# Kernel optimization log

Hardware: AMD Instinct MI355X
Metric: run time of the kernel (lower is better)

## Reference

```python
import jax, jax.numpy as jnp
import numpy as np

N, E, C, H, EDGE_DIM, HID = 50000, 800000, 128, 8, 64, 512
D = C // H  # head dim = out_channels_conv


def layer_norm(x, g, b, eps=1e-5):
    mu = x.mean(-1, keepdims=True)
    var = ((x - mu) ** 2).mean(-1, keepdims=True)
    return (x - mu) * jax.lax.rsqrt(var + eps) * g + b


def _lin_init(k, fan_in, fan_out):
    s = 1.0 / np.sqrt(fan_in)
    kw, kb = jax.random.split(k)
    w = jax.random.uniform(kw, (fan_in, fan_out), minval=-s, maxval=s, dtype=jnp.float32)
    b = jax.random.uniform(kb, (fan_out,), minval=-s, maxval=s, dtype=jnp.float32)
    return w, b


def setup_inputs() -> dict:
    key = jax.random.key(0)
    ks = jax.random.split(key, 16)
    wq, bq = _lin_init(ks[0], C, C)
    wk, bk = _lin_init(ks[1], C, C)
    wv, bv = _lin_init(ks[2], C, C)
    ws, bs = _lin_init(ks[3], C, C)          # lin_self
    we, be = _lin_init(ks[4], EDGE_DIM, C)   # lin_edge
    wp, bp = _lin_init(ks[5], C, C)          # projection
    w1, b1 = _lin_init(ks[6], C, HID)        # node_dst_mlp[0]
    w2, b2 = _lin_init(ks[7], HID, C)        # node_dst_mlp[2]
    x = jax.random.normal(ks[8], (N, C), dtype=jnp.float32)
    edge_attr = jax.random.normal(ks[9], (E, EDGE_DIM), dtype=jnp.float32)
    edge_index = jax.random.randint(ks[10], (2, E), 0, N, dtype=jnp.int64)
    return dict(
        x=x, edge_attr=edge_attr, edge_index=edge_index,
        wq=wq, bq=bq, wk=wk, bk=bk, wv=wv, bv=bv, ws=ws, bs=bs,
        we=we, be=be, wp=wp, bp=bp, w1=w1, b1=b1, w2=w2, b2=b2,
        ln1_g=jnp.ones((C,), jnp.float32), ln1_b=jnp.zeros((C,), jnp.float32),
        ln2_g=jnp.ones((C,), jnp.float32), ln2_b=jnp.zeros((C,), jnp.float32),
    )


def reference(x, edge_attr, edge_index,
              wq, bq, wk, bk, wv, bv, ws, bs, we, be, wp, bp,
              w1, b1, w2, b2, ln1_g, ln1_b, ln2_g, ln2_b):
    src, dst = edge_index[0], edge_index[1]

    x_skip = x
    xn = layer_norm(x, ln1_g, ln1_b)                       # layer_norm_attention
    x_r = xn @ ws + bs                                     # lin_self residual
    q = (xn @ wq + bq).reshape(N, H, D)
    k = (xn @ wk + bk).reshape(N, H, D)
    v = (xn @ wv + bv).reshape(N, H, D)
    e = (edge_attr @ we + be).reshape(E, H, D)             # lin_edge (edge_pre_mlp = Identity)

    # edge-indexed multi-head attention: softmax over incoming edges per dst node
    ke = k[src] + e                                        # [E,H,D]
    alpha = jnp.einsum('ehd,ehd->eh', q[dst], ke) / np.sqrt(D)   # [E,H]
    amax = jax.lax.stop_gradient(jax.ops.segment_max(alpha, dst, num_segments=N))
    ex = jnp.exp(alpha - amax[dst])
    den = jax.ops.segment_sum(ex, dst, num_segments=N)
    w = ex / (den[dst] + 1e-16)                            # [E,H]
    out = jax.ops.segment_sum(w[:, :, None] * (v[src] + e), dst, num_segments=N)  # [N,H,D]
    out = out.reshape(N, C)

    out = (out + x_r) @ wp + bp                            # projection
    out = out + x_skip
    h = layer_norm(out, ln2_g, ln2_b)                      # layer_norm_mlp_dst
    h = jax.nn.gelu(h @ w1 + b1) @ w2 + b2                 # node_dst_mlp
    nodes_new = out + h
    return nodes_new, edge_attr
```

## Files before the change

kernel.cpp:

```cpp
#include <hip/hip_runtime.h>
#include <hip/hip_bf16.h>
#include <cstdio>

#define NN 50000
#define NE 800000
#define CC 128
#define EDIM 64
#define HIDN 512

using bf16 = __hip_bfloat16;
typedef short sh8 __attribute__((ext_vector_type(8)));
typedef float f32x4 __attribute__((ext_vector_type(4)));

static __device__ __forceinline__ float b2f(bf16 v){ return __bfloat162float(v); }
static __device__ __forceinline__ bf16 f2b(float v){ return __float2bfloat16(v); }
static __device__ __forceinline__ float u2f(unsigned short u){
    union { unsigned int i; float f; } w; w.i = ((unsigned int)u) << 16; return w.f;
}
static __device__ __forceinline__ unsigned short f2u(float f){
    bf16 b = __float2bfloat16(f);
    return *reinterpret_cast<unsigned short*>(&b);
}
static __device__ __forceinline__ float2 loadbf2(const bf16* p){
    __hip_bfloat162 v = *reinterpret_cast<const __hip_bfloat162*>(p);
    return make_float2(__bfloat162float(v.x), __bfloat162float(v.y));
}
static __device__ __forceinline__ float gelu_tanh(float x){
    const float c = 0.7978845608028654f;
    float u = c * (x + 0.044715f * x * x * x);
    return x / (1.0f + __expf(-2.0f * u));
}

constexpr size_t AL(size_t x){ return (x + 255) & ~(size_t)255; }
constexpr size_t OFF_FLAG = 0;
constexpr size_t OFF_DEG  = 256;
constexpr size_t OFF_ROW  = AL(OFF_DEG + (size_t)(NN + 1) * 4);
constexpr size_t OFF_CUR  = AL(OFF_ROW + (size_t)(NN + 1) * 4);
constexpr size_t OFF_SRC  = AL(OFF_CUR + (size_t)(NN + 1) * 4);
constexpr size_t OFF_DST  = AL(OFF_SRC + (size_t)NE * 4);
constexpr size_t OFF_QC   = AL(OFF_DST + (size_t)NE * 4);
constexpr size_t OFF_KC   = AL(OFF_QC  + (size_t)NN * CC * 2);
constexpr size_t OFF_VC   = AL(OFF_KC  + (size_t)NN * CC * 2);
constexpr size_t OFF_ATT  = AL(OFF_VC  + (size_t)NN * CC * 2);
constexpr size_t OFF_PRM  = AL(OFF_ATT + (size_t)NN * CC * 2);
constexpr size_t PRM_ELEMS = 4*(16384+128) + 8192+128 + 16384+128 + 65536+512 + 65536+128 + 4*128;
constexpr size_t OFF_ALP  = AL(OFF_PRM + PRM_ELEMS * 2);
constexpr size_t OFF_VP   = AL(OFF_ALP + (size_t)NE * 8 * 2);
constexpr size_t OFF_XRC  = AL(OFF_VP + (size_t)NE * CC * 2);
constexpr size_t OFF_WFQ  = AL(OFF_XRC + (size_t)NN * CC * 2);
constexpr size_t OFF_WFK  = OFF_WFQ + 32768;
constexpr size_t OFF_WFV  = OFF_WFK + 32768;
constexpr size_t OFF_WFS  = OFF_WFV + 32768;
constexpr size_t OFF_WFP  = OFF_WFS + 32768;
constexpr size_t OFF_WF1  = OFF_WFP + 32768;
constexpr size_t OFF_WF2  = OFF_WF1 + 131072;
constexpr size_t OFF_WFE  = OFF_WF2 + 131072;
constexpr size_t OFF_BSUM = OFF_WFE + 16384;
constexpr size_t WS_NEED  = OFF_BSUM + 256;

__global__ void k_detect(const unsigned short* xw, const unsigned int* ew, int* flags){
    __shared__ int sw, sz;
    if (threadIdx.x == 0){ sw = 0; sz = 0; }
    __syncthreads();
    int w = 0;
    for (int i = threadIdx.x; i < 8192; i += 256){
        unsigned e = (xw[i] >> 7) & 0xFF;
        if (e == 0xFF || (e != 0 && (e < 0x60 || e > 0x90))) w++;
    }
    atomicAdd(&sw, w);
    int z = 0;
    for (int i = threadIdx.x; i < 2048; i += 256)
        if (ew[2*i+1] == 0u) z++;
    atomicAdd(&sz, z);
    __syncthreads();
    if (threadIdx.x == 0){
        flags[0] = (sw > 2048) ? 1 : 0;
        flags[1] = (sz > 1536) ? 1 : 0;
    }
}

struct CvtJob { const void* s; bf16* d; int n; };
struct CvtJobs { CvtJob j[20]; };
__global__ void k_cvt_all(CvtJobs jobs, const int* flags){
    const int f = flags[0];
    const int e = blockIdx.x >> 5;
    const CvtJob J = jobs.j[e];
    const int stride = 32 * 256;
    for (int i = (blockIdx.x & 31) * 256 + threadIdx.x; i < J.n; i += stride){
        if (f) J.d[i] = f2b(((const float*)J.s)[i]);
        else   J.d[i] = ((const bf16*)J.s)[i];
    }
}

__global__ void k_cvt_idx(const int* e32, int* srcI, int* dstI, int* deg, const int* flags){
    const int f = flags[1];
    int i = blockIdx.x * blockDim.x + threadIdx.x;
    const int stride = gridDim.x * blockDim.x;
    if (f){
        const long long* e64 = (const long long*)e32;
        for (; i < NE; i += stride){
            srcI[i] = (int)e64[i];
            const int d = (int)e64[NE + i];
            dstI[i] = d;
            atomicAdd(&deg[d], 1);
        }
    } else {
        for (; i < NE; i += stride){
            srcI[i] = e32[i];
            const int d = e32[NE + i];
            dstI[i] = d;
            atomicAdd(&deg[d], 1);
        }
    }
}

struct WJob { const bf16* W; bf16* WF; int K; int N; };
struct WJobs { WJob j[8]; };
__global__ void k_wprep_all(WJobs jobs){
    const WJob J = jobs.j[blockIdx.x / 48];
    const int KS = J.K >> 5;
    const int total = J.K * J.N;
    for (int o = (blockIdx.x % 48) * 256 + threadIdx.x; o < total; o += 48 * 256){
        const int j  = o & 7;
        const int ln = (o >> 3) & 63;
        const int tt = o >> 9;
        const int ks = tt % KS, ct = tt / KS;
        const int kk = (ks << 5) + ((ln >> 4) << 3) + j;
        const int c  = (ct << 4) + (ln & 15);
        J.WF[o] = J.W[kk * J.N + c];
    }
}

#define ASWZ(row, chunk)  (((row) << 8)  + ((((chunk) ^ ((row) & 15))) << 4))
#define HSWZ(row, chunk)  (((row) << 10) + ((((chunk) ^ ((row) & 15))) << 4))
#define EASWZ(row, chunk) (((row) << 7)  + ((((chunk) ^ ((row) & 7)))  << 4))

static __device__ __forceinline__ void gemm_nodes_128(
    const unsigned short* Abase, int row0, int lane,
    const bf16* __restrict__ WF, const bf16* __restrict__ bias,
    bf16* __restrict__ outp, int n0)
{
    const int rA = row0 + (lane & 15);
    sh8 af[4];
    #pragma unroll
    for (int ks = 0; ks < 4; ++ks)
        af[ks] = *(const sh8*)((const char*)Abase + ASWZ(rA, (ks << 2) + (lane >> 4)));
    f32x4 acc[8] = {};
    #pragma unroll
    for (int ks = 0; ks < 4; ++ks)
        #pragma unroll
        for (int ct = 0; ct < 8; ++ct){
            sh8 bfr = *(const sh8*)(WF + ((size_t)((ct << 2) + ks) * 64 + lane) * 8);
            acc[ct] = __builtin_amdgcn_mfma_f32_16x16x32_bf16(af[ks], bfr, acc[ct], 0, 0, 0);
        }
    #pragma unroll
    for (int ct = 0; ct < 8; ++ct){
        const int c = (ct << 4) + (lane & 15);
        const float bv = b2f(bias[c]);
        #pragma unroll
        for (int i = 0; i < 4; ++i){
            const int r = row0 + ((lane >> 4) << 2) + i;
            if (n0 + r < NN)
                outp[(size_t)(n0 + r) * CC + c] = f2b(acc[ct][i] + bv);
        }
    }
}

__global__ __launch_bounds__(256) void k_node_pre2(
    const void* __restrict__ x_raw, const int* __restrict__ flags,
    const bf16* __restrict__ WFq, const bf16* __restrict__ bq,
    const bf16* __restrict__ WFk, const bf16* __restrict__ bk,
    const bf16* __restrict__ WFv, const bf16* __restrict__ bv,
    const bf16* __restrict__ WFs, const bf16* __restrict__ bs,
    const bf16* __restrict__ g,  const bf16* __restrict__ bb,
    bf16* __restrict__ q, bf16* __restrict__ k, bf16* __restrict__ v,
    bf16* __restrict__ xr)
{
    __shared__ unsigned short A[64 * 128];
    const int t = threadIdx.x, lane = t & 63, wid = t >> 6;
    const int n0 = blockIdx.x * 64;

    if (flags[0]){
        const float* x = (const float*)x_raw;
        #pragma unroll
        for (int it = 0; it < 8; ++it){
            const int u = t + 256 * it;
            const int row = u >> 5, c = (u & 31) << 2;
            float4 a = make_float4(0.f, 0.f, 0.f, 0.f);
            if (n0 + row < NN)
                a = *(const float4*)&x[(size_t)(n0 + row) * CC + c];
            ushort4 b;
            b.x = f2u(a.x); b.y = f2u(a.y); b.z = f2u(a.z); b.w = f2u(a.w);
            *(ushort4*)((char*)A + ASWZ(row, c >> 3) + ((c & 7) << 1)) = b;
        }
    } else {
        const bf16* x = (const bf16*)x_raw;
        #pragma unroll
        for (int it = 0; it < 4; ++it){
            const int c8 = t + 256 * it;
            const int row = c8 >> 4, chunk = c8 & 15, col = chunk << 3;
            uint4 val = make_uint4(0u, 0u, 0u, 0u);
            if (n0 + row < NN)
                val = *(const uint4*)&x[(size_t)(n0 + row) * CC + col];
            *(uint4*)((char*)A + ASWZ(row, chunk)) = val;
        }
    }
    __syncthreads();

    {
        const int nd = wid * 16 + (lane & 15), qd = lane >> 4;
        float vals[32];
        #pragma unroll
        for (int i = 0; i < 4; ++i){
            uint4 u = *(const uint4*)((const char*)A + ASWZ(nd, (qd << 2) + i));
            unsigned uu[4] = {u.x, u.y, u.z, u.w};
            #pragma unroll
            for (int j2 = 0; j2 < 4; ++j2){
                vals[i*8 + j2*2]     = u2f((unsigned short)(uu[j2] & 0xFFFF));
                vals[i*8 + j2*2 + 1] = u2f((unsigned short)(uu[j2] >> 16));
            }
        }
        float s = 0.f;
        #pragma unroll
        for (int i = 0; i < 32; ++i) s += vals[i];
        s += __shfl_xor(s, 16); s += __shfl_xor(s, 32);
        const float mu = s * (1.0f / CC);
        float vv = 0.f;
        #pragma unroll
        for (int i = 0; i < 32; ++i){ const float d = vals[i] - mu; vv += d * d; }
        vv += __shfl_xor(vv, 16); vv += __shfl_xor(vv, 32);
        const float rstd = rsqrtf(vv * (1.0f / CC) + 1e-5f);
        #pragma unroll
        for (int i = 0; i < 4; ++i){
            unsigned w[4];
            #pragma unroll
            for (int j2 = 0; j2 < 4; ++j2){
                const int c0 = qd * 32 + i * 8 + j2 * 2;
                const float a0 = (vals[i*8+j2*2]   - mu) * rstd * b2f(g[c0])   + b2f(bb[c0]);
                const float a1 = (vals[i*8+j2*2+1] - mu) * rstd * b2f(g[c0+1]) + b2f(bb[c0+1]);
                w[j2] = (unsigned)f2u(a0) | ((unsigned)f2u(a1) << 16);
            }
            *(uint4*)((char*)A + ASWZ(nd, (qd << 2) + i)) = make_uint4(w[0], w[1], w[2], w[3]);
        }
    }
    __syncthreads();

    const int row0 = wid * 16;
    gemm_nodes_128(A, row0, lane, WFq, bq, q,  n0);
    gemm_nodes_128(A, row0, lane, WFk, bk, k,  n0);
    gemm_nodes_128(A, row0, lane, WFv, bv, v,  n0);
    gemm_nodes_128(A, row0, lane, WFs, bs, xr, n0);
}

__global__ __launch_bounds__(1024) void k_scan1(const int* __restrict__ deg,
                                                int* __restrict__ row, int* __restrict__ bsum){
    __shared__ int sb[1024];
    const int t = threadIdx.x;
    const int idx = blockIdx.x * 1024 + t;
    sb[t] = (idx < NN) ? deg[idx] : 0;
    __syncthreads();
    for (int off = 1; off < 1024; off <<= 1){
        int tv = (t >= off) ? sb[t - off] : 0;
        __syncthreads();
        sb[t] += tv;
        __syncthreads();
    }
    if (idx < NN) row[idx + 1] = sb[t];
    if (t == 1023) bsum[blockIdx.x] = sb[1023];
}

__global__ __launch_bounds__(1024) void k_scan3(const int* __restrict__ bsum,
                                                int* __restrict__ row, int* __restrict__ cur){
    __shared__ int sadd;
    const int t = threadIdx.x;
    if (t < 64){
        int a = 0;
        for (int i = t; i < (int)blockIdx.x; i += 64) a += bsum[i];
        for (int off = 32; off; off >>= 1) a += __shfl_xor(a, off);
        if (t == 0) sadd = a;
    }
    __syncthreads();
    const int idx = blockIdx.x * 1024 + t;
    if (idx < NN){
        const int vfin = row[idx + 1] + sadd;
        row[idx + 1] = vfin;
        cur[idx + 1] = vfin;
    }
    if (idx == 0){ row[0] = 0; cur[0] = 0; }
}

__global__ __launch_bounds__(256) void k_edge4(
    const void* __restrict__ ea_raw, const int* __restrict__ flags,
    const bf16* __restrict__ WFe, const bf16* __restrict__ be,
    const bf16* __restrict__ kv_q, const bf16* __restrict__ kv_k, const bf16* __restrict__ kv_v,
    const int* __restrict__ srcI, const int* __restrict__ dstI, int* __restrict__ cur,
    unsigned short* __restrict__ alphap, unsigned short* __restrict__ vperm,
    void* __restrict__ outv)
{
    __shared__ unsigned short EA[64 * 64];
    __shared__ unsigned short ET[64 * 128];
    const int t = threadIdx.x, lane = t & 63, wid = t >> 6;
    const int e0 = blockIdx.x * 64;

    if (flags[0]){
        const float* ea = (const float*)ea_raw;
        float* outd = (float*)outv + (size_t)NN * CC;
        #pragma unroll
        for (int it = 0; it < 4; ++it){
            const int u = t + 256 * it;
            const int row = u >> 4, c = (u & 15) << 2;
            const size_t o = (size_t)(e0 + row) * EDIM + c;
            const float4 a = *(const float4*)&ea[o];
            *(float4*)&outd[o] = a;
            ushort4 b;
            b.x = f2u(a.x); b.y = f2u(a.y); b.z = f2u(a.z); b.w = f2u(a.w);
            *(ushort4*)((char*)EA + EASWZ(row, c >> 3) + ((c & 7) << 1)) = b;
        }
    } else {
        const unsigned short* ea = (const unsigned short*)ea_raw;
        unsigned short* outd = (unsigned short*)outv + (size_t)NN * CC;
        #pragma unroll
        for (int it = 0; it < 2; ++it){
            const int u = t + 256 * it;
            const int row = u >> 3, c = (u & 7) << 3;
            const size_t o = (size_t)(e0 + row) * EDIM + c;
            uint4 raw = *(const uint4*)&ea[o];
            *(uint4*)&outd[o] = raw;
            *(uint4*)((char*)EA + EASWZ(row, c >> 3)) = raw;
        }
    }
    __syncthreads();

    const int row0 = wid * 16;
    {
        const int rA = row0 + (lane & 15);
        sh8 af[2];
        #pragma unroll
        for (int ks = 0; ks < 2; ++ks)
            af[ks] = *(const sh8*)((const char*)EA + EASWZ(rA, (ks << 2) + (lane >> 4)));
        f32x4 acc[8] = {};
        #pragma unroll
        for (int ks = 0; ks < 2; ++ks)
            #pragma unroll
            for (int ct = 0; ct < 8; ++ct){
                sh8 bfr = *(const sh8*)(WFe + ((size_t)((ct << 1) + ks) * 64 + lane) * 8);
                acc[ct] = __builtin_amdgcn_mfma_f32_16x16x32_bf16(af[ks], bfr, acc[ct], 0, 0, 0);
            }
        #pragma unroll
        for (int ct = 0; ct < 8; ++ct){
            const int c = (ct << 4) + (lane & 15);
            const float bv = b2f(be[c]);
            #pragma unroll
            for (int i = 0; i < 4; ++i){
                const int r = row0 + ((lane >> 4) << 2) + i;
                *(unsigned short*)((char*)ET + ASWZ(r, c >> 3) + ((c & 7) << 1)) =
                    f2u(acc[ct][i] + bv);
            }
        }
    }
    __syncthreads();

    const int g = t >> 5, cT = t & 31, c = cT << 2;
    int s8[8], d8[8];
    #pragma unroll
    for (int i = 0; i < 8; ++i){
        const int eid = e0 + g * 8 + i;
        s8[i] = srcI[eid];
        d8[i] = dstI[eid];
    }
    int pmine = 0;
    if (cT < 8) pmine = atomicAdd(&cur[dstI[e0 + g * 8 + cT]], 1);
    int p8[8];
    #pragma unroll
    for (int i = 0; i < 8; ++i)
        p8[i] = __shfl(pmine, ((g & 1) << 5) + i);

    ushort4 kr[8], vr[8], qr[8];
    #pragma unroll
    for (int i = 0; i < 8; ++i) kr[i] = *(const ushort4*)&kv_k[(size_t)s8[i] * CC + c];
    #pragma unroll
    for (int i = 0; i < 8; ++i) vr[i] = *(const ushort4*)&kv_v[(size_t)s8[i] * CC + c];
    #pragma unroll
    for (int i = 0; i < 8; ++i) qr[i] = *(const ushort4*)&kv_q[(size_t)d8[i] * CC + c];
    #pragma unroll
    for (int i = 0; i < 8; ++i){
        const ushort4 ev = *(const ushort4*)((const char*)ET + ASWZ(g * 8 + i, c >> 3) + ((c & 7) << 1));
        const float e0_ = u2f(ev.x), e1_ = u2f(ev.y), e2_ = u2f(ev.z), e3_ = u2f(ev.w);
        float part = u2f(qr[i].x) * (e0_ + u2f(kr[i].x)) + u2f(qr[i].y) * (e1_ + u2f(kr[i].y))
                   + u2f(qr[i].z) * (e2_ + u2f(kr[i].z)) + u2f(qr[i].w) * (e3_ + u2f(kr[i].w));
        part += __shfl_xor(part, 1);
        part += __shfl_xor(part, 2);
        if ((cT & 3) == 0)
            alphap[(size_t)p8[i] * 8 + (cT >> 2)] = f2u(part * 0.25f);
        ushort4 vo;
        vo.x = f2u(e0_ + u2f(vr[i].x)); vo.y = f2u(e1_ + u2f(vr[i].y));
        vo.z = f2u(e2_ + u2f(vr[i].z)); vo.w = f2u(e3_ + u2f(vr[i].w));
        *(ushort4*)&vperm[(size_t)p8[i] * CC + c] = vo;
    }
}

__global__ __launch_bounds__(256) void k_attn3(
    const unsigned short* __restrict__ alphap, const bf16* __restrict__ vperm,
    const int* __restrict__ rowstart, bf16* __restrict__ attn_bf)
{
    const int t = threadIdx.x, lane = t & 63, wid = t >> 6;
    const int n = blockIdx.x * 4 + wid;
    const int h = lane >> 3;

    float m = -INFINITY, den = 0.0f;
    float2 num = make_float2(0.0f, 0.0f);

    const int jb = rowstart[n], je = rowstart[n + 1];
    for (int j = jb; j < je; ++j) {
        const float alpha = u2f(alphap[(size_t)j * 8 + h]);
        const float2 v2 = loadbf2(&vperm[(size_t)j * CC + 2 * lane]);
        if (alpha > m) {
            const float sc = __expf(m - alpha);
            den *= sc; num.x *= sc; num.y *= sc;
            m = alpha;
        }
        const float p = __expf(alpha - m);
        den += p;
        num.x += p * v2.x;
        num.y += p * v2.y;
    }
    const float inv = 1.0f / (den + 1e-16f);
    __hip_bfloat162 pr;
    pr.x = f2b(num.x * inv);
    pr.y = f2b(num.y * inv);
    *reinterpret_cast<__hip_bfloat162*>(&attn_bf[(size_t)n * CC + 2 * lane]) = pr;
}

__global__ __launch_bounds__(256) void k_post2(
    const bf16* __restrict__ attn_bf, const bf16* __restrict__ xr,
    const void* __restrict__ x_raw,
    const bf16* __restrict__ WFp, const bf16* __restrict__ bp,
    const bf16* __restrict__ WF1, const bf16* __restrict__ b1,
    const bf16* __restrict__ WF2, const bf16* __restrict__ b2c,
    const bf16* __restrict__ g2, const bf16* __restrict__ bb2,
    void* __restrict__ outv, const int* __restrict__ flags)
{
    __shared__ unsigned short A[64 * 128];
    __shared__ unsigned short HID[64 * 512];
    const int t = threadIdx.x, lane = t & 63, wid = t >> 6;
    const int n0 = blockIdx.x * 64;
    const int f32io = flags[0];

    #pragma unroll
    for (int it = 0; it < 4; ++it){
        const int c8 = t + 256 * it;
        const int row = c8 >> 4, chunk = c8 & 15, col = chunk << 3;
        unsigned w[4] = {0u, 0u, 0u, 0u};
        if (n0 + row < NN){
            const size_t o = (size_t)(n0 + row) * CC + col;
            uint4 a4 = *(const uint4*)&attn_bf[o];
            uint4 r4 = *(const uint4*)&xr[o];
            unsigned au[4] = {a4.x, a4.y, a4.z, a4.w};
            unsigned ru[4] = {r4.x, r4.y, r4.z, r4.w};
            #pragma unroll
            for (int j2 = 0; j2 < 4; ++j2){
                const float lo = u2f((unsigned short)(au[j2] & 0xFFFF)) +
                                 u2f((unsigned short)(ru[j2] & 0xFFFF));
                const float hi = u2f((unsigned short)(au[j2] >> 16)) +
                                 u2f((unsigned short)(ru[j2] >> 16));
                w[j2] = (unsigned)f2u(lo) | ((unsigned)f2u(hi) << 16);
            }
        }
        *(uint4*)((char*)A + ASWZ(row, chunk)) = make_uint4(w[0], w[1], w[2], w[3]);
    }
    __syncthreads();

    const int row0 = wid * 16;
    const int rA = row0 + (lane & 15);

    float out2[8][4];
    {
        sh8 af[4];
        #pragma unroll
        for (int ks = 0; ks < 4; ++ks)
            af[ks] = *(const sh8*)((const char*)A + ASWZ(rA, (ks << 2) + (lane >> 4)));
        f32x4 acc[8] = {};
        #pragma unroll
        for (int ks = 0; ks < 4; ++ks)
            #pragma unroll
            for (int ct = 0; ct < 8; ++ct){
                sh8 bfr = *(const sh8*)(WFp + ((size_t)((ct << 2) + ks) * 64 + lane) * 8);
                acc[ct] = __builtin_amdgcn_mfma_f32_16x16x32_bf16(af[ks], bfr, acc[ct], 0, 0, 0);
            }
        #pragma unroll
        for (int ct = 0; ct < 8; ++ct){
            const int c = (ct << 4) + (lane & 15);
            const float bv = b2f(bp[c]);
            #pragma unroll
            for (int i = 0; i < 4; ++i){
                const int r = row0 + ((lane >> 4) << 2) + i;
                float xs = 0.f;
                if (n0 + r < NN){
                    const size_t o = (size_t)(n0 + r) * CC + c;
                    xs = f32io ? ((const float*)x_raw)[o] : b2f(((const bf16*)x_raw)[o]);
                }
                out2[ct][i] = acc[ct][i] + bv + xs;
            }
        }
    }

    {
        float mu[4], rstd[4];
        #pragma unroll
        for (int i = 0; i < 4; ++i){
            float s = 0.f;
            #pragma unroll
            for (int ct = 0; ct < 8; ++ct) s += out2[ct][i];
            s += __shfl_xor(s, 1); s += __shfl_xor(s, 2);
            s += __shfl_xor(s, 4); s += __shfl_xor(s, 8);
            mu[i] = s * (1.0f / CC);
        }
        #pragma unroll
        for (int i = 0; i < 4; ++i){
            float vv = 0.f;
            #pragma unroll
            for (int ct = 0; ct < 8; ++ct){ const float d = out2[ct][i] - mu[i]; vv += d * d; }
            vv += __shfl_xor(vv, 1); vv += __shfl_xor(vv, 2);
            vv += __shfl_xor(vv, 4); vv += __shfl_xor(vv, 8);
            rstd[i] = rsqrtf(vv * (1.0f / CC) + 1e-5f);
        }
        #pragma unroll
        for (int ct = 0; ct < 8; ++ct){
            const int c = (ct << 4) + (lane & 15);
            const float gv = b2f(g2[c]), bbv = b2f(bb2[c]);
            const int chunk = c >> 3;
            #pragma unroll
            for (int i = 0; i < 4; ++i){
                const int r = row0 + ((lane >> 4) << 2) + i;
                const float ln = (out2[ct][i] - mu[i]) * rstd[i] * gv + bbv;
                *(unsigned short*)((char*)A + ASWZ(r, chunk) + ((c & 7) << 1)) = f2u(ln);
            }
        }
    }

    {
        sh8 af[4];
        #pragma unroll
        for (int ks = 0; ks < 4; ++ks)
            af[ks] = *(const sh8*)((const char*)A + ASWZ(rA, (ks << 2) + (lane >> 4)));
        #pragma unroll
        for (int grp = 0; grp < 4; ++grp){
            f32x4 acc[8] = {};
            #pragma unroll
            for (int ks = 0; ks < 4; ++ks)
                #pragma unroll
                for (int ctl = 0; ctl < 8; ++ctl){
                    const int ct = grp * 8 + ctl;
                    sh8 bfr = *(const sh8*)(WF1 + ((size_t)((ct << 2) + ks) * 64 + lane) * 8);
                    acc[ctl] = __builtin_amdgcn_mfma_f32_16x16x32_bf16(af[ks], bfr, acc[ctl], 0, 0, 0);
                }
            #pragma unroll
            for (int ctl = 0; ctl < 8; ++ctl){
                const int ct = grp * 8 + ctl;
                const int c = (ct << 4) + (lane & 15);
                const float bv = b2f(b1[c]);
                const int chunk = c >> 3;
                #pragma unroll
                for (int i = 0; i < 4; ++i){
                    const int r = row0 + ((lane >> 4) << 2) + i;
                    const float h = gelu_tanh(acc[ctl][i] + bv);
                    *(unsigned short*)((char*)HID + HSWZ(r, chunk) + ((c & 7) << 1)) = f2u(h);
                }
            }
        }
    }

    {
        f32x4 acc[8] = {};
        #pragma unroll
        for (int ks = 0; ks < 16; ++ks){
            sh8 afh = *(const sh8*)((const char*)HID + HSWZ(rA, (ks << 2) + (lane >> 4)));
            #pragma unroll
            for (int ct = 0; ct < 8; ++ct){
                sh8 bfr = *(const sh8*)(WF2 + ((size_t)((ct << 4) + ks) * 64 + lane) * 8);
                acc[ct] = __builtin_amdgcn_mfma_f32_16x16x32_bf16(afh, bfr, acc[ct], 0, 0, 0);
            }
        }
        #pragma unroll
        for (int ct = 0; ct < 8; ++ct){
            const int c = (ct << 4) + (lane & 15);
            const float bv = b2f(b2c[c]);
            #pragma unroll
            for (int i = 0; i < 4; ++i){
                const int r = row0 + ((lane >> 4) << 2) + i;
                if (n0 + r < NN){
                    const float val = out2[ct][i] + acc[ct][i] + bv;
                    if (f32io) ((float*)outv)[(size_t)(n0 + r) * CC + c] = val;
                    else       ((bf16*)outv)[(size_t)(n0 + r) * CC + c] = f2b(val);
                }
            }
        }
    }
}

extern "C" void kernel_launch(void* const* d_in, const int* in_sizes, int n_in,
                              void* d_out, int out_size, void* d_ws, size_t ws_size,
                              hipStream_t stream)
{
    if (ws_size < WS_NEED) {
        fprintf(stderr, "[kl] WS TOO SMALL ws=%zu need=%zu\n", ws_size, WS_NEED);
        return;
    }

    char* ws = (char*)d_ws;
    int*  flags = (int*)(ws + OFF_FLAG);
    int*  deg   = (int*)(ws + OFF_DEG);
    int*  row   = (int*)(ws + OFF_ROW);
    int*  cur   = (int*)(ws + OFF_CUR);
    int*  srcI  = (int*)(ws + OFF_SRC);
    int*  dstI  = (int*)(ws + OFF_DST);
    int*  bsum  = (int*)(ws + OFF_BSUM);
    bf16* qC    = (bf16*)(ws + OFF_QC);
    bf16* kC    = (bf16*)(ws + OFF_KC);
    bf16* vC    = (bf16*)(ws + OFF_VC);
    bf16* attC  = (bf16*)(ws + OFF_ATT);
    bf16* xrC   = (bf16*)(ws + OFF_XRC);
    unsigned short* alphap = (unsigned short*)(ws + OFF_ALP);
    unsigned short* vperm  = (unsigned short*)(ws + OFF_VP);
    bf16* WFq = (bf16*)(ws + OFF_WFQ);
    bf16* WFk = (bf16*)(ws + OFF_WFK);
    bf16* WFv = (bf16*)(ws + OFF_WFV);
    bf16* WFs = (bf16*)(ws + OFF_WFS);
    bf16* WFp = (bf16*)(ws + OFF_WFP);
    bf16* WF1 = (bf16*)(ws + OFF_WF1);
    bf16* WF2 = (bf16*)(ws + OFF_WF2);
    bf16* WFe = (bf16*)(ws + OFF_WFE);

    bf16* P = (bf16*)(ws + OFF_PRM);
    bf16 *wqC=P; P+=16384; bf16 *bqC=P; P+=128;
    bf16 *wkC=P; P+=16384; bf16 *bkC=P; P+=128;
    bf16 *wvC=P; P+=16384; bf16 *bvC=P; P+=128;
    bf16 *wsC=P; P+=16384; bf16 *bsC=P; P+=128;
    bf16 *weC=P; P+=8192;  bf16 *beC=P; P+=128;
    bf16 *wpC=P; P+=16384; bf16 *bpC=P; P+=128;
    bf16 *w1C=P; P+=65536; bf16 *b1C=P; P+=512;
    bf16 *w2C=P; P+=65536; bf16 *b2C=P; P+=128;
    bf16 *g1C=P; P+=128;   bf16 *n1C=P; P+=128;
    bf16 *g2C=P; P+=128;   bf16 *n2C=P; P+=128;

    hipMemsetAsync(deg, 0, (size_t)(NN + 1) * sizeof(int), stream);

    k_detect<<<1, 256, 0, stream>>>((const unsigned short*)d_in[0],
                                    (const unsigned int*)d_in[2], flags);

    {
        CvtJobs cj;
        bf16* dsts[20] = {wqC,bqC,wkC,bkC,wvC,bvC,wsC,bsC,weC,beC,
                          wpC,bpC,w1C,b1C,w2C,b2C,g1C,n1C,g2C,n2C};
        const int ns[20] = {16384,128,16384,128,16384,128,16384,128,8192,128,
                            16384,128,65536,512,65536,128,128,128,128,128};
        for (int i = 0; i < 20; ++i){ cj.j[i].s = d_in[3 + i]; cj.j[i].d = dsts[i]; cj.j[i].n = ns[i]; }
        k_cvt_all<<<20 * 32, 256, 0, stream>>>(cj, flags);
    }
    k_cvt_idx<<<1024, 256, 0, stream>>>((const int*)d_in[2], srcI, dstI, deg, flags);

    {
        WJobs wj;
        const WJob js[8] = {{wqC,WFq,128,128},{wkC,WFk,128,128},{wvC,WFv,128,128},
                            {wsC,WFs,128,128},{wpC,WFp,128,128},{w1C,WF1,128,512},
                            {w2C,WF2,512,128},{weC,WFe,64,128}};
        for (int i = 0; i < 8; ++i) wj.j[i] = js[i];
        k_wprep_all<<<8 * 48, 256, 0, stream>>>(wj);
    }

    const int NB64 = (NN + 63) / 64;
    const int NSC  = (NN + 1023) / 1024;
    k_node_pre2<<<NB64, 256, 0, stream>>>(d_in[0], flags, WFq, bqC, WFk, bkC, WFv, bvC,
                                          WFs, bsC, g1C, n1C, qC, kC, vC, xrC);
    k_scan1<<<NSC, 1024, 0, stream>>>(deg, row, bsum);
    k_scan3<<<NSC, 1024, 0, stream>>>(bsum, row, cur);
    k_edge4<<<NE / 64, 256, 0, stream>>>(d_in[1], flags, WFe, beC, qC, kC, vC,
                                         srcI, dstI, cur, alphap, vperm, d_out);
    k_attn3<<<NN / 4, 256, 0, stream>>>(alphap, (const bf16*)vperm, row, attC);
    k_post2<<<NB64, 256, 0, stream>>>(attC, xrC, d_in[0], WFp, bpC, WF1, b1C, WF2, b2C,
                                      g2C, n2C, d_out, flags);
}
```

Measured before the change: 505.8 us.

## Interleave K/V rows, hoist edge gathers before edge GEMM, fuse weight conversion

K and V projections are now written into one interleaved [N,256] buffer, so each edge's source gather reads K and V from the same 512-byte row. The index loads, atomic slot reservation and K/V/Q gathers in the edge kernel are moved ahead of the edge-attribute GEMM, so their memory latency overlaps with the MFMA work. Weight dtype conversion is folded into the weight-relayout kernel, which removes the intermediate bf16 weight copies and shrinks the conversion launch to biases only. The hoisted gathers hold many more live registers through the GEMM, which may lower occupancy.

```diff
diff --git a/kernel.cpp b/kernel.cpp
--- a/kernel.cpp
+++ b/kernel.cpp
@@ -39,11 +39,10 @@
 constexpr size_t OFF_SRC  = AL(OFF_CUR + (size_t)(NN + 1) * 4);
 constexpr size_t OFF_DST  = AL(OFF_SRC + (size_t)NE * 4);
 constexpr size_t OFF_QC   = AL(OFF_DST + (size_t)NE * 4);
-constexpr size_t OFF_KC   = AL(OFF_QC  + (size_t)NN * CC * 2);
-constexpr size_t OFF_VC   = AL(OFF_KC  + (size_t)NN * CC * 2);
-constexpr size_t OFF_ATT  = AL(OFF_VC  + (size_t)NN * CC * 2);
+constexpr size_t OFF_KV   = AL(OFF_QC  + (size_t)NN * CC * 2);
+constexpr size_t OFF_ATT  = AL(OFF_KV  + (size_t)NN * 256 * 2);
 constexpr size_t OFF_PRM  = AL(OFF_ATT + (size_t)NN * CC * 2);
-constexpr size_t PRM_ELEMS = 4*(16384+128) + 8192+128 + 16384+128 + 65536+512 + 65536+128 + 4*128;
+constexpr size_t PRM_ELEMS = 4096;
 constexpr size_t OFF_ALP  = AL(OFF_PRM + PRM_ELEMS * 2);
 constexpr size_t OFF_VP   = AL(OFF_ALP + (size_t)NE * 8 * 2);
 constexpr size_t OFF_XRC  = AL(OFF_VP + (size_t)NE * CC * 2);
@@ -80,13 +79,13 @@
 }
 
 struct CvtJob { const void* s; bf16* d; int n; };
-struct CvtJobs { CvtJob j[20]; };
+struct CvtJobs { CvtJob j[12]; };
 __global__ void k_cvt_all(CvtJobs jobs, const int* flags){
     const int f = flags[0];
-    const int e = blockIdx.x >> 5;
+    const int e = blockIdx.x >> 1;
     const CvtJob J = jobs.j[e];
-    const int stride = 32 * 256;
-    for (int i = (blockIdx.x & 31) * 256 + threadIdx.x; i < J.n; i += stride){
+    const int stride = 2 * 256;
+    for (int i = (blockIdx.x & 1) * 256 + threadIdx.x; i < J.n; i += stride){
         if (f) J.d[i] = f2b(((const float*)J.s)[i]);
         else   J.d[i] = ((const bf16*)J.s)[i];
     }
@@ -114,9 +113,10 @@
     }
 }
 
-struct WJob { const bf16* W; bf16* WF; int K; int N; };
+struct WJob { const void* W; bf16* WF; int K; int N; };
 struct WJobs { WJob j[8]; };
-__global__ void k_wprep_all(WJobs jobs){
+__global__ void k_wprep_all(WJobs jobs, const int* flags){
+    const int f = flags[0];
     const WJob J = jobs.j[blockIdx.x / 48];
     const int KS = J.K >> 5;
     const int total = J.K * J.N;
@@ -127,7 +127,8 @@
         const int ks = tt % KS, ct = tt / KS;
         const int kk = (ks << 5) + ((ln >> 4) << 3) + j;
         const int c  = (ct << 4) + (ln & 15);
-        J.WF[o] = J.W[kk * J.N + c];
+        const int src = kk * J.N + c;
+        J.WF[o] = f ? f2b(((const float*)J.W)[src]) : ((const bf16*)J.W)[src];
     }
 }
 
@@ -138,7 +139,7 @@
 static __device__ __forceinline__ void gemm_nodes_128(
     const unsigned short* Abase, int row0, int lane,
     const bf16* __restrict__ WF, const bf16* __restrict__ bias,
-    bf16* __restrict__ outp, int n0)
+    bf16* __restrict__ outp, int n0, int ostride, int ocol)
 {
     const int rA = row0 + (lane & 15);
     sh8 af[4];
@@ -161,7 +162,7 @@
         for (int i = 0; i < 4; ++i){
             const int r = row0 + ((lane >> 4) << 2) + i;
             if (n0 + r < NN)
-                outp[(size_t)(n0 + r) * CC + c] = f2b(acc[ct][i] + bv);
+                outp[(size_t)(n0 + r) * ostride + ocol + c] = f2b(acc[ct][i] + bv);
         }
     }
 }
@@ -173,8 +174,7 @@
     const bf16* __restrict__ WFv, const bf16* __restrict__ bv,
     const bf16* __restrict__ WFs, const bf16* __restrict__ bs,
     const bf16* __restrict__ g,  const bf16* __restrict__ bb,
-    bf16* __restrict__ q, bf16* __restrict__ k, bf16* __restrict__ v,
-    bf16* __restrict__ xr)
+    bf16* __restrict__ q, bf16* __restrict__ kv, bf16* __restrict__ xr)
 {
     __shared__ unsigned short A[64 * 128];
     const int t = threadIdx.x, lane = t & 63, wid = t >> 6;
@@ -246,10 +246,10 @@
     __syncthreads();
 
     const int row0 = wid * 16;
-    gemm_nodes_128(A, row0, lane, WFq, bq, q,  n0);
-    gemm_nodes_128(A, row0, lane, WFk, bk, k,  n0);
-    gemm_nodes_128(A, row0, lane, WFv, bv, v,  n0);
-    gemm_nodes_128(A, row0, lane, WFs, bs, xr, n0);
+    gemm_nodes_128(A, row0, lane, WFq, bq, q,  n0, CC,  0);
+    gemm_nodes_128(A, row0, lane, WFk, bk, kv, n0, 256, 0);
+    gemm_nodes_128(A, row0, lane, WFv, bv, kv, n0, 256, 128);
+    gemm_nodes_128(A, row0, lane, WFs, bs, xr, n0, CC,  0);
 }
 
 __global__ __launch_bounds__(1024) void k_scan1(const int* __restrict__ deg,
@@ -289,10 +289,10 @@
     if (idx == 0){ row[0] = 0; cur[0] = 0; }
 }
 
-__global__ __launch_bounds__(256) void k_edge4(
+__global__ __launch_bounds__(256) void k_edge5(
     const void* __restrict__ ea_raw, const int* __restrict__ flags,
     const bf16* __restrict__ WFe, const bf16* __restrict__ be,
-    const bf16* __restrict__ kv_q, const bf16* __restrict__ kv_k, const bf16* __restrict__ kv_v,
+    const bf16* __restrict__ kv_q, const bf16* __restrict__ kvKV,
     const int* __restrict__ srcI, const int* __restrict__ dstI, int* __restrict__ cur,
     unsigned short* __restrict__ alphap, unsigned short* __restrict__ vperm,
     void* __restrict__ outv)
@@ -301,6 +301,28 @@
     __shared__ unsigned short ET[64 * 128];
     const int t = threadIdx.x, lane = t & 63, wid = t >> 6;
     const int e0 = blockIdx.x * 64;
+    const int g = t >> 5, cT = t & 31, c = cT << 2;
+
+    int s8[8], d8[8];
+    #pragma unroll
+    for (int i = 0; i < 8; ++i){
+        const int eid = e0 + g * 8 + i;
+        s8[i] = srcI[eid];
+        d8[i] = dstI[eid];
+    }
+    int pmine = 0;
+    if (cT < 8) pmine = atomicAdd(&cur[dstI[e0 + g * 8 + cT]], 1);
+    ushort4 kr[8], vr[8], qr[8];
+    #pragma unroll
+    for (int i = 0; i < 8; ++i) kr[i] = *(const ushort4*)&kvKV[(size_t)s8[i] * 256 + c];
+    #pragma unroll
+    for (int i = 0; i < 8; ++i) vr[i] = *(const ushort4*)&kvKV[(size_t)s8[i] * 256 + 128 + c];
+    #pragma unroll
+    for (int i = 0; i < 8; ++i) qr[i] = *(const ushort4*)&kv_q[(size_t)d8[i] * CC + c];
+    int p8[8];
+    #pragma unroll
+    for (int i = 0; i < 8; ++i)
+        p8[i] = __shfl(pmine, ((g & 1) << 5) + i);
 
     if (flags[0]){
         const float* ea = (const float*)ea_raw;
@@ -308,13 +330,13 @@
         #pragma unroll
         for (int it = 0; it < 4; ++it){
             const int u = t + 256 * it;
-            const int row = u >> 4, c = (u & 15) << 2;
-            const size_t o = (size_t)(e0 + row) * EDIM + c;
+            const int row = u >> 4, cc2 = (u & 15) << 2;
+            const size_t o = (size_t)(e0 + row) * EDIM + cc2;
             const float4 a = *(const float4*)&ea[o];
             *(float4*)&outd[o] = a;
             ushort4 b;
             b.x = f2u(a.x); b.y = f2u(a.y); b.z = f2u(a.z); b.w = f2u(a.w);
-            *(ushort4*)((char*)EA + EASWZ(row, c >> 3) + ((c & 7) << 1)) = b;
+            *(ushort4*)((char*)EA + EASWZ(row, cc2 >> 3) + ((cc2 & 7) << 1)) = b;
         }
     } else {
         const unsigned short* ea = (const unsigned short*)ea_raw;
@@ -322,11 +344,11 @@
         #pragma unroll
         for (int it = 0; it < 2; ++it){
             const int u = t + 256 * it;
-            const int row = u >> 3, c = (u & 7) << 3;
-            const size_t o = (size_t)(e0 + row) * EDIM + c;
+            const int row = u >> 3, cc2 = (u & 7) << 3;
+            const size_t o = (size_t)(e0 + row) * EDIM + cc2;
             uint4 raw = *(const uint4*)&ea[o];
             *(uint4*)&outd[o] = raw;
-            *(uint4*)((char*)EA + EASWZ(row, c >> 3)) = raw;
+            *(uint4*)((char*)EA + EASWZ(row, cc2 >> 3)) = raw;
         }
     }
     __syncthreads();
@@ -348,40 +370,18 @@
             }
         #pragma unroll
         for (int ct = 0; ct < 8; ++ct){
-            const int c = (ct << 4) + (lane & 15);
-            const float bv = b2f(be[c]);
+            const int cc3 = (ct << 4) + (lane & 15);
+            const float bv = b2f(be[cc3]);
             #pragma unroll
             for (int i = 0; i < 4; ++i){
                 const int r = row0 + ((lane >> 4) << 2) + i;
-                *(unsigned short*)((char*)ET + ASWZ(r, c >> 3) + ((c & 7) << 1)) =
+                *(unsigned short*)((char*)ET + ASWZ(r, cc3 >> 3) + ((cc3 & 7) << 1)) =
                     f2u(acc[ct][i] + bv);
             }
         }
     }
     __syncthreads();
 
-    const int g = t >> 5, cT = t & 31, c = cT << 2;
-    int s8[8], d8[8];
-    #pragma unroll
-    for (int i = 0; i < 8; ++i){
-        const int eid = e0 + g * 8 + i;
-        s8[i] = srcI[eid];
-        d8[i] = dstI[eid];
-    }
-    int pmine = 0;
-    if (cT < 8) pmine = atomicAdd(&cur[dstI[e0 + g * 8 + cT]], 1);
-    int p8[8];
-    #pragma unroll
-    for (int i = 0; i < 8; ++i)
-        p8[i] = __shfl(pmine, ((g & 1) << 5) + i);
-
-    ushort4 kr[8], vr[8], qr[8];
-    #pragma unroll
-    for (int i = 0; i < 8; ++i) kr[i] = *(const ushort4*)&kv_k[(size_t)s8[i] * CC + c];
-    #pragma unroll
-    for (int i = 0; i < 8; ++i) vr[i] = *(const ushort4*)&kv_v[(size_t)s8[i] * CC + c];
-    #pragma unroll
-    for (int i = 0; i < 8; ++i) qr[i] = *(const ushort4*)&kv_q[(size_t)d8[i] * CC + c];
     #pragma unroll
     for (int i = 0; i < 8; ++i){
         const ushort4 ev = *(const ushort4*)((const char*)ET + ASWZ(g * 8 + i, c >> 3) + ((c & 7) << 1));
@@ -616,8 +616,7 @@
     int*  dstI  = (int*)(ws + OFF_DST);
     int*  bsum  = (int*)(ws + OFF_BSUM);
     bf16* qC    = (bf16*)(ws + OFF_QC);
-    bf16* kC    = (bf16*)(ws + OFF_KC);
-    bf16* vC    = (bf16*)(ws + OFF_VC);
+    bf16* kvC   = (bf16*)(ws + OFF_KV);
     bf16* attC  = (bf16*)(ws + OFF_ATT);
     bf16* xrC   = (bf16*)(ws + OFF_XRC);
     unsigned short* alphap = (unsigned short*)(ws + OFF_ALP);
@@ -632,16 +631,12 @@
     bf16* WFe = (bf16*)(ws + OFF_WFE);
 
     bf16* P = (bf16*)(ws + OFF_PRM);
-    bf16 *wqC=P; P+=16384; bf16 *bqC=P; P+=128;
-    bf16 *wkC=P; P+=16384; bf16 *bkC=P; P+=128;
-    bf16 *wvC=P; P+=16384; bf16 *bvC=P; P+=128;
-    bf16 *wsC=P; P+=16384; bf16 *bsC=P; P+=128;
-    bf16 *weC=P; P+=8192;  bf16 *beC=P; P+=128;
-    bf16 *wpC=P; P+=16384; bf16 *bpC=P; P+=128;
-    bf16 *w1C=P; P+=65536; bf16 *b1C=P; P+=512;
-    bf16 *w2C=P; P+=65536; bf16 *b2C=P; P+=128;
-    bf16 *g1C=P; P+=128;   bf16 *n1C=P; P+=128;
-    bf16 *g2C=P; P+=128;   bf16 *n2C=P; P+=128;
+    bf16 *bqC=P; P+=128; bf16 *bkC=P; P+=128;
+    bf16 *bvC=P; P+=128; bf16 *bsC=P; P+=128;
+    bf16 *beC=P; P+=128; bf16 *bpC=P; P+=128;
+    bf16 *b1C=P; P+=512; bf16 *b2C=P; P+=128;
+    bf16 *g1C=P; P+=128; bf16 *n1C=P; P+=128;
+    bf16 *g2C=P; P+=128; bf16 *n2C=P; P+=128;
 
     hipMemsetAsync(deg, 0, (size_t)(NN + 1) * sizeof(int), stream);
 
@@ -650,31 +645,30 @@
 
     {
         CvtJobs cj;
-        bf16* dsts[20] = {wqC,bqC,wkC,bkC,wvC,bvC,wsC,bsC,weC,beC,
-                          wpC,bpC,w1C,b1C,w2C,b2C,g1C,n1C,g2C,n2C};
-        const int ns[20] = {16384,128,16384,128,16384,128,16384,128,8192,128,
-                            16384,128,65536,512,65536,128,128,128,128,128};
-        for (int i = 0; i < 20; ++i){ cj.j[i].s = d_in[3 + i]; cj.j[i].d = dsts[i]; cj.j[i].n = ns[i]; }
-        k_cvt_all<<<20 * 32, 256, 0, stream>>>(cj, flags);
+        bf16* dsts[12] = {bqC,bkC,bvC,bsC,beC,bpC,b1C,b2C,g1C,n1C,g2C,n2C};
+        const int idxs[12] = {4,6,8,10,12,14,16,18,19,20,21,22};
+        const int ns[12]   = {128,128,128,128,128,128,512,128,128,128,128,128};
+        for (int i = 0; i < 12; ++i){ cj.j[i].s = d_in[idxs[i]]; cj.j[i].d = dsts[i]; cj.j[i].n = ns[i]; }
+        k_cvt_all<<<12 * 2, 256, 0, stream>>>(cj, flags);
     }
     k_cvt_idx<<<1024, 256, 0, stream>>>((const int*)d_in[2], srcI, dstI, deg, flags);
 
     {
         WJobs wj;
-        const WJob js[8] = {{wqC,WFq,128,128},{wkC,WFk,128,128},{wvC,WFv,128,128},
-                            {wsC,WFs,128,128},{wpC,WFp,128,128},{w1C,WF1,128,512},
-                            {w2C,WF2,512,128},{weC,WFe,64,128}};
+        const WJob js[8] = {{d_in[3],WFq,128,128},{d_in[5],WFk,128,128},{d_in[7],WFv,128,128},
+                            {d_in[9],WFs,128,128},{d_in[13],WFp,128,128},{d_in[15],WF1,128,512},
+                            {d_in[17],WF2,512,128},{d_in[11],WFe,64,128}};
         for (int i = 0; i < 8; ++i) wj.j[i] = js[i];
-        k_wprep_all<<<8 * 48, 256, 0, stream>>>(wj);
+        k_wprep_all<<<8 * 48, 256, 0, stream>>>(wj, flags);
     }
 
     const int NB64 = (NN + 63) / 64;
     const int NSC  = (NN + 1023) / 1024;
     k_node_pre2<<<NB64, 256, 0, stream>>>(d_in[0], flags, WFq, bqC, WFk, bkC, WFv, bvC,
-                                          WFs, bsC, g1C, n1C, qC, kC, vC, xrC);
+                                          WFs, bsC, g1C, n1C, qC, kvC, xrC);
     k_scan1<<<NSC, 1024, 0, stream>>>(deg, row, bsum);
     k_scan3<<<NSC, 1024, 0, stream>>>(bsum, row, cur);
-    k_edge4<<<NE / 64, 256, 0, stream>>>(d_in[1], flags, WFe, beC, qC, kC, vC,
+    k_edge5<<<NE / 64, 256, 0, stream>>>(d_in[1], flags, WFe, beC, qC, kvC,
                                          srcI, dstI, cur, alphap, vperm, d_out);
     k_attn3<<<NN / 4, 256, 0, stream>>>(alphap, (const bf16*)vperm, row, attC);
     k_post2<<<NB64, 256, 0, stream>>>(attC, xrC, d_in[0], WFp, bpC, WF1, b1C, WF2, b2C,
```

Result: slower. 532.9 us (+5.4%).
